# Kernel optimization log

Hardware: AMD Instinct MI355X
Metric: run time of the kernel (lower is better)

The kernel has to match this reference:

```python
import jax, jax.numpy as jnp
import numpy as np

N = 50000       # nodes
E = 100000      # edges (avg degree ~2 per direction, molecular graphs)
EDGE_DIM = 8
EH = 32         # edge-MLP hidden width
DIN = 32
H1, H2 = 32, 64
NGRAPH = 256
EPS = 1e-5


def setup_inputs():
    key = jax.random.key(0)
    ks = jax.random.split(key, 16)
    def rn(k, shape, fan):
        return jax.random.normal(k, shape, jnp.float32) * np.float32(1.0 / np.sqrt(fan))
    return {
        "x": jax.random.normal(ks[0], (N, DIN), jnp.float32),
        "edge_index": jax.random.randint(ks[1], (2, E), 0, N),
        "edge_attr": jax.random.uniform(ks[2], (E, EDGE_DIM), jnp.float32),
        "batch_index": jnp.sort(jax.random.randint(ks[3], (N,), 0, NGRAPH)),
        # NNConv layer 1: DIN -> H1
        "e1_w1": rn(ks[4], (EDGE_DIM, EH), EDGE_DIM), "e1_b1": jnp.zeros((EH,), jnp.float32),
        "e1_w2": rn(ks[5], (EH, DIN * H1), EH), "e1_b2": jnp.zeros((DIN * H1,), jnp.float32),
        "root1": rn(ks[6], (DIN, H1), DIN), "bias1": jnp.zeros((H1,), jnp.float32),
        # NNConv layer 2: H1 -> H2
        "e2_w1": rn(ks[7], (EDGE_DIM, EH), EDGE_DIM), "e2_b1": jnp.zeros((EH,), jnp.float32),
        "e2_w2": rn(ks[8], (EH, H1 * H2), EH), "e2_b2": jnp.zeros((H1 * H2,), jnp.float32),
        "root2": rn(ks[9], (H1, H2), H1), "bias2": jnp.zeros((H2,), jnp.float32),
        # MLP head
        "h1_w": rn(ks[10], (2 * H2, H2), 2 * H2), "h1_b": jnp.zeros((H2,), jnp.float32),
        "bn1_g": jnp.ones((H2,), jnp.float32), "bn1_b": jnp.zeros((H2,), jnp.float32),
        "bn1_m": jnp.zeros((H2,), jnp.float32), "bn1_v": jnp.ones((H2,), jnp.float32),
        "h2_w": rn(ks[11], (H2, H2 // 2), H2), "h2_b": jnp.zeros((H2 // 2,), jnp.float32),
        "bn2_g": jnp.ones((H2 // 2,), jnp.float32), "bn2_b": jnp.zeros((H2 // 2,), jnp.float32),
        "bn2_m": jnp.zeros((H2 // 2,), jnp.float32), "bn2_v": jnp.ones((H2 // 2,), jnp.float32),
        "h3_w": rn(ks[12], (H2 // 2, 1), H2 // 2), "h3_b": jnp.zeros((1,), jnp.float32),
    }


def nnconv_layer(x, src, dst, edge_attr, w1, b1, w2, b2, root, bias, din, dout):
    # edge MLP -> per-edge weight matrix [E, din, dout]
    h = jax.nn.relu(edge_attr @ w1 + b1)
    W = (h @ w2 + b2).reshape(-1, din, dout)
    # gather source features, per-edge matmul, scatter-add to targets
    msg = jnp.einsum('ei,eio->eo', x[src], W)
    agg = jax.ops.segment_sum(msg, dst, num_segments=x.shape[0])
    return x @ root + agg + bias


def bn_eval(x, g, b, m, v):
    return (x - m) * jax.lax.rsqrt(v + EPS) * g + b


def reference(x, edge_index, edge_attr, batch_index,
              e1_w1, e1_b1, e1_w2, e1_b2, root1, bias1,
              e2_w1, e2_b1, e2_w2, e2_b2, root2, bias2,
              h1_w, h1_b, bn1_g, bn1_b, bn1_m, bn1_v,
              h2_w, h2_b, bn2_g, bn2_b, bn2_m, bn2_v,
              h3_w, h3_b):
    src, dst = edge_index[0], edge_index[1]
    h = nnconv_layer(x, src, dst, edge_attr, e1_w1, e1_b1, e1_w2, e1_b2, root1, bias1, DIN, H1)
    h = jax.nn.relu(h)
    h = nnconv_layer(h, src, dst, edge_attr, e2_w1, e2_b1, e2_w2, e2_b2, root2, bias2, H1, H2)
    # global max + mean pool per graph
    gmax = jax.ops.segment_max(h, batch_index, num_segments=NGRAPH)
    cnt = jax.ops.segment_sum(jnp.ones((h.shape[0],), h.dtype), batch_index, num_segments=NGRAPH)
    gmean = jax.ops.segment_sum(h, batch_index, num_segments=NGRAPH) / jnp.maximum(cnt, 1.0)[:, None]
    feat = jnp.concatenate([gmax, gmean], axis=1)  # [NGRAPH, 2*H2]
    # MLP head (eval mode: BN uses running stats, dropout = identity)
    z = jax.nn.relu(bn_eval(feat @ h1_w + h1_b, bn1_g, bn1_b, bn1_m, bn1_v))
    z = jax.nn.relu(bn_eval(z @ h2_w + h2_b, bn2_g, bn2_b, bn2_m, bn2_v))
    return z @ h3_w + h3_b
```

## Files before the change

### kernel.cpp

```cpp
#include <hip/hip_runtime.h>
#include <hip/hip_fp16.h>

#define N_NODES 50000
#define N_EDGES 100000
#define EDGE_DIM 8
#define EHID 32
#define DIN 32
#define H1 32
#define H2 64
#define NGRAPH 256
#define BN_EPS 1e-5f
#define KTOT 1056

#define EH_BLOCKS  ((N_EDGES + 255) / 256)
#define PREP_TOTAL ((H1 + H2) * KTOT)
#define PREP_BLOCKS (PREP_TOTAL / 256)
#define INIT_BLOCKS 253
#define MSG_BLOCKS 512

typedef __attribute__((ext_vector_type(8))) _Float16 f16x8;
typedef __attribute__((ext_vector_type(4))) float f32x4;
typedef unsigned int uint32;

__device__ inline void atomicMaxF(float* addr, float v) {
    if (v >= 0.0f) atomicMax((int*)addr, __float_as_int(v));
    else           atomicMin((unsigned int*)addr, __float_as_uint(v));
}

__device__ inline uint32 pk_f16(float a, float b) {
    uint32 r;
    asm("v_cvt_pkrtz_f16_f32 %0, %1, %2" : "=v"(r) : "v"(a), "v"(b));
    return r;
}

union GF { uint32 u[4]; f16x8 v; };

__device__ inline f16x8 mul_h(uint32 h, const GF& g) {
    GF r;
    asm("v_pk_mul_f16 %0, %1, %2" : "=v"(r.u[0]) : "v"(h), "v"(g.u[0]));
    asm("v_pk_mul_f16 %0, %1, %2" : "=v"(r.u[1]) : "v"(h), "v"(g.u[1]));
    asm("v_pk_mul_f16 %0, %1, %2" : "=v"(r.u[2]) : "v"(h), "v"(g.u[2]));
    asm("v_pk_mul_f16 %0, %1, %2" : "=v"(r.u[3]) : "v"(h), "v"(g.u[3]));
    return r.v;
}

__global__ __launch_bounds__(256) void prologue_kernel(
    const float* __restrict__ edge_attr,
    const float* __restrict__ e1w1, const float* __restrict__ e1b1,
    const float* __restrict__ e2w1, const float* __restrict__ e2b1,
    const float* __restrict__ e1w2, const float* __restrict__ e1b2,
    const float* __restrict__ e2w2, const float* __restrict__ e2b2,
    uint32* __restrict__ hpk1, uint32* __restrict__ hpk2,
    unsigned short* __restrict__ w2h1, unsigned short* __restrict__ w2h2,
    float* __restrict__ agg1, float* __restrict__ agg2,
    float* __restrict__ gmax, float* __restrict__ gsum, float* __restrict__ gcnt)
{
    int bid = blockIdx.x, tid = threadIdx.x;
    if (bid < EH_BLOCKS) {
        __shared__ float s_w[2][EDGE_DIM * EHID];
        __shared__ float s_b[2][EHID];
        if (tid < EDGE_DIM * EHID) { s_w[0][tid] = e1w1[tid]; s_w[1][tid] = e2w1[tid]; }
        if (tid < EHID) { s_b[0][tid] = e1b1[tid]; s_b[1][tid] = e2b1[tid]; }
        __syncthreads();
        int e = bid * 256 + tid;
        if (e >= N_EDGES) return;
        const float4* eap = reinterpret_cast<const float4*>(edge_attr + (size_t)e * EDGE_DIM);
        float4 v0 = eap[0], v1 = eap[1];
        float ea[EDGE_DIM] = {v0.x, v0.y, v0.z, v0.w, v1.x, v1.y, v1.z, v1.w};
#pragma unroll
        for (int L = 0; L < 2; ++L) {
            uint32* hp = (L == 0 ? hpk1 : hpk2) + (size_t)e * EHID;
#pragma unroll
            for (int k4 = 0; k4 < EHID; k4 += 4) {
                uint32 t[4];
#pragma unroll
                for (int q = 0; q < 4; ++q) {
                    int k = k4 + q;
                    float acc = s_b[L][k];
#pragma unroll
                    for (int j = 0; j < EDGE_DIM; ++j) acc += ea[j] * s_w[L][j * EHID + k];
                    acc = fmaxf(acc, 0.0f);
                    t[q] = pk_f16(acc, acc);
                }
                uint4 r; r.x = t[0]; r.y = t[1]; r.z = t[2]; r.w = t[3];
                *reinterpret_cast<uint4*>(hp + k4) = r;
            }
        }
    } else if (bid < EH_BLOCKS + PREP_BLOCKS) {
        int idx = (bid - EH_BLOCKS) * 256 + tid;
        const int n1 = H1 * KTOT;
        if (idx < n1) {
            int o = idx / KTOT, k = idx % KTOT;
            float v = (k < EHID * DIN) ? e1w2[(k >> 5) * (DIN * H1) + (k & 31) * H1 + o]
                                       : e1b2[(k - EHID * DIN) * H1 + o];
            w2h1[idx] = __half_as_ushort(__float2half(v));
        } else {
            int j = idx - n1;
            int o = j / KTOT, k = j % KTOT;
            float v = (k < EHID * DIN) ? e2w2[(k >> 5) * (DIN * H2) + (k & 31) * H2 + o]
                                       : e2b2[(k - EHID * DIN) * H2 + o];
            w2h2[j] = __half_as_ushort(__float2half(v));
        }
    } else {
        int lb = bid - EH_BLOCKS - PREP_BLOCKS;
        int stride = INIT_BLOCKS * 256;
        int i0 = lb * 256 + tid;
        for (int i = i0; i < N_NODES * H1; i += stride) agg1[i] = 0.0f;
        for (int i = i0; i < N_NODES * H2; i += stride) agg2[i] = 0.0f;
        for (int i = i0; i < NGRAPH * H2; i += stride) { gmax[i] = __int_as_float(0xff800000); gsum[i] = 0.0f; }
        for (int i = i0; i < NGRAPH; i += stride) gcnt[i] = 0.0f;
    }
}

template <int DOUT>
__global__ __launch_bounds__(256, 2) void msg_v4_kernel(
    const float* __restrict__ gsrc,
    const uint32* __restrict__ hpk,
    const int* __restrict__ src, const int* __restrict__ dst,
    const unsigned short* __restrict__ w2h,
    float* __restrict__ agg)
{
    constexpr int NT = DOUT / 16;
    __shared__ __align__(16) uint32 hlds[4][2][32][36];

    const int tid = threadIdx.x;
    const int wave = tid >> 6;
    const int lane = tid & 63;
    const int col = lane & 15;
    const int kq = lane >> 4;

    const int w = blockIdx.x * 4 + wave;
    const int ot = w % NT;
    int it = w / NT;
    const int strideIt = (MSG_BLOCKS * 4) / NT;
    const int NIT = N_EDGES / 32;

    f16x8 B[33];
    {
        const unsigned short* bp = w2h + (size_t)(ot * 16 + col) * KTOT + kq * 8;
#pragma unroll
        for (int kk = 0; kk < 33; ++kk)
            B[kk] = *reinterpret_cast<const f16x8*>(bp + kk * 32);
    }
    if (it >= NIT) return;

    int buf = 0;

    int e0 = it * 32;
    int sA = src[e0 + col], sB = src[e0 + 16 + col];
    float4 gA0 = *reinterpret_cast<const float4*>(gsrc + (size_t)sA * DIN + kq * 8);
    float4 gA1 = *reinterpret_cast<const float4*>(gsrc + (size_t)sA * DIN + kq * 8 + 4);
    float4 gB0 = *reinterpret_cast<const float4*>(gsrc + (size_t)sB * DIN + kq * 8);
    float4 gB1 = *reinterpret_cast<const float4*>(gsrc + (size_t)sB * DIN + kq * 8 + 4);
    uint4 hA0 = *reinterpret_cast<const uint4*>(hpk + (size_t)(e0 + col) * EHID + kq * 8);
    uint4 hA1 = *reinterpret_cast<const uint4*>(hpk + (size_t)(e0 + col) * EHID + kq * 8 + 4);
    uint4 hB0 = *reinterpret_cast<const uint4*>(hpk + (size_t)(e0 + 16 + col) * EHID + kq * 8);
    uint4 hB1 = *reinterpret_cast<const uint4*>(hpk + (size_t)(e0 + 16 + col) * EHID + kq * 8 + 4);
    int4 ddA = *reinterpret_cast<const int4*>(dst + e0 + kq * 4);
    int4 ddB = *reinterpret_cast<const int4*>(dst + e0 + 16 + kq * 4);

    int it1 = it + strideIt;
    int s1A = 0, s1B = 0;
    if (it1 < NIT) { s1A = src[it1 * 32 + col]; s1B = src[it1 * 32 + 16 + col]; }

    GF gfA, gfB;
    gfA.u[0] = pk_f16(gA0.x, gA0.y); gfA.u[1] = pk_f16(gA0.z, gA0.w);
    gfA.u[2] = pk_f16(gA1.x, gA1.y); gfA.u[3] = pk_f16(gA1.z, gA1.w);
    gfB.u[0] = pk_f16(gB0.x, gB0.y); gfB.u[1] = pk_f16(gB0.z, gB0.w);
    gfB.u[2] = pk_f16(gB1.x, gB1.y); gfB.u[3] = pk_f16(gB1.z, gB1.w);
    *reinterpret_cast<uint4*>(&hlds[wave][0][col][kq * 8])          = hA0;
    *reinterpret_cast<uint4*>(&hlds[wave][0][col][kq * 8 + 4])      = hA1;
    *reinterpret_cast<uint4*>(&hlds[wave][0][16 + col][kq * 8])     = hB0;
    *reinterpret_cast<uint4*>(&hlds[wave][0][16 + col][kq * 8 + 4]) = hB1;

    for (;;) {
        int it2 = it1 + strideIt;
        int s2A = 0, s2B = 0;
        if (it2 < NIT) { s2A = src[it2 * 32 + col]; s2B = src[it2 * 32 + 16 + col]; }

        const bool nv = (it1 < NIT);
        float4 ngA0, ngA1, ngB0, ngB1;
        uint4 nhA0, nhA1, nhB0, nhB1;
        int4 nddA, nddB;
        if (nv) {
            int ne0 = it1 * 32;
            ngA0 = *reinterpret_cast<const float4*>(gsrc + (size_t)s1A * DIN + kq * 8);
            ngA1 = *reinterpret_cast<const float4*>(gsrc + (size_t)s1A * DIN + kq * 8 + 4);
            ngB0 = *reinterpret_cast<const float4*>(gsrc + (size_t)s1B * DIN + kq * 8);
            ngB1 = *reinterpret_cast<const float4*>(gsrc + (size_t)s1B * DIN + kq * 8 + 4);
            nhA0 = *reinterpret_cast<const uint4*>(hpk + (size_t)(ne0 + col) * EHID + kq * 8);
            nhA1 = *reinterpret_cast<const uint4*>(hpk + (size_t)(ne0 + col) * EHID + kq * 8 + 4);
            nhB0 = *reinterpret_cast<const uint4*>(hpk + (size_t)(ne0 + 16 + col) * EHID + kq * 8);
            nhB1 = *reinterpret_cast<const uint4*>(hpk + (size_t)(ne0 + 16 + col) * EHID + kq * 8 + 4);
            nddA = *reinterpret_cast<const int4*>(dst + ne0 + kq * 4);
            nddB = *reinterpret_cast<const int4*>(dst + ne0 + 16 + kq * 4);
        }

        f32x4 accA = (f32x4){0.f, 0.f, 0.f, 0.f};
        f32x4 accB = (f32x4){0.f, 0.f, 0.f, 0.f};
#pragma unroll
        for (int t = 0; t < 8; ++t) {
            uint4 ha = *reinterpret_cast<const uint4*>(&hlds[wave][buf][col][t * 4]);
            uint4 hb = *reinterpret_cast<const uint4*>(&hlds[wave][buf][16 + col][t * 4]);
            accA = __builtin_amdgcn_mfma_f32_16x16x32_f16(mul_h(ha.x, gfA), B[t * 4 + 0], accA, 0, 0, 0);
            accB = __builtin_amdgcn_mfma_f32_16x16x32_f16(mul_h(hb.x, gfB), B[t * 4 + 0], accB, 0, 0, 0);
            accA = __builtin_amdgcn_mfma_f32_16x16x32_f16(mul_h(ha.y, gfA), B[t * 4 + 1], accA, 0, 0, 0);
            accB = __builtin_amdgcn_mfma_f32_16x16x32_f16(mul_h(hb.y, gfB), B[t * 4 + 1], accB, 0, 0, 0);
            accA = __builtin_amdgcn_mfma_f32_16x16x32_f16(mul_h(ha.z, gfA), B[t * 4 + 2], accA, 0, 0, 0);
            accB = __builtin_amdgcn_mfma_f32_16x16x32_f16(mul_h(hb.z, gfB), B[t * 4 + 2], accB, 0, 0, 0);
            accA = __builtin_amdgcn_mfma_f32_16x16x32_f16(mul_h(ha.w, gfA), B[t * 4 + 3], accA, 0, 0, 0);
            accB = __builtin_amdgcn_mfma_f32_16x16x32_f16(mul_h(hb.w, gfB), B[t * 4 + 3], accB, 0, 0, 0);
        }
        accA = __builtin_amdgcn_mfma_f32_16x16x32_f16(gfA.v, B[32], accA, 0, 0, 0);
        accB = __builtin_amdgcn_mfma_f32_16x16x32_f16(gfB.v, B[32], accB, 0, 0, 0);

        atomicAdd(&agg[(size_t)ddA.x * DOUT + ot * 16 + col], accA[0]);
        atomicAdd(&agg[(size_t)ddA.y * DOUT + ot * 16 + col], accA[1]);
        atomicAdd(&agg[(size_t)ddA.z * DOUT + ot * 16 + col], accA[2]);
        atomicAdd(&agg[(size_t)ddA.w * DOUT + ot * 16 + col], accA[3]);
        atomicAdd(&agg[(size_t)ddB.x * DOUT + ot * 16 + col], accB[0]);
        atomicAdd(&agg[(size_t)ddB.y * DOUT + ot * 16 + col], accB[1]);
        atomicAdd(&agg[(size_t)ddB.z * DOUT + ot * 16 + col], accB[2]);
        atomicAdd(&agg[(size_t)ddB.w * DOUT + ot * 16 + col], accB[3]);

        if (!nv) break;

        buf ^= 1;
        *reinterpret_cast<uint4*>(&hlds[wave][buf][col][kq * 8])          = nhA0;
        *reinterpret_cast<uint4*>(&hlds[wave][buf][col][kq * 8 + 4])      = nhA1;
        *reinterpret_cast<uint4*>(&hlds[wave][buf][16 + col][kq * 8])     = nhB0;
        *reinterpret_cast<uint4*>(&hlds[wave][buf][16 + col][kq * 8 + 4]) = nhB1;
        gfA.u[0] = pk_f16(ngA0.x, ngA0.y); gfA.u[1] = pk_f16(ngA0.z, ngA0.w);
        gfA.u[2] = pk_f16(ngA1.x, ngA1.y); gfA.u[3] = pk_f16(ngA1.z, ngA1.w);
        gfB.u[0] = pk_f16(ngB0.x, ngB0.y); gfB.u[1] = pk_f16(ngB0.z, ngB0.w);
        gfB.u[2] = pk_f16(ngB1.x, ngB1.y); gfB.u[3] = pk_f16(ngB1.z, ngB1.w);
        ddA = nddA; ddB = nddB;
        s1A = s2A; s1B = s2B;
        it = it1; it1 = it2;
    }
}

template <int DOUTN, bool RELU>
__global__ __launch_bounds__(256) void node_update_kernel(
    const float* __restrict__ in, const float* __restrict__ root,
    const float* __restrict__ agg, const float* __restrict__ bias,
    float* __restrict__ out)
{
    constexpr int NPB = 256 / DOUTN;
    __shared__ float roots[DIN * DOUTN];
    __shared__ float ins[NPB][DIN + 1];
    int tid = threadIdx.x;
    for (int idx = tid; idx < DIN * DOUTN; idx += 256) roots[idx] = root[idx];
    int o = tid % DOUTN, nl = tid / DOUTN;
    float bo = bias[o];
    const int nchunks = (N_NODES + NPB - 1) / NPB;
    for (int c = blockIdx.x; c < nchunks; c += gridDim.x) {
        int nBase = c * NPB;
        __syncthreads();
        for (int idx = tid; idx < NPB * DIN; idx += 256) {
            int nn = nBase + idx / DIN;
            ins[idx / DIN][idx % DIN] = (nn < N_NODES) ? in[(size_t)nn * DIN + (idx % DIN)] : 0.0f;
        }
        __syncthreads();
        int n = nBase + nl;
        if (n < N_NODES) {
            float t = agg[(size_t)n * DOUTN + o] + bo;
#pragma unroll
            for (int i = 0; i < DIN; ++i) t += ins[nl][i] * roots[i * DOUTN + o];
            if (RELU) t = fmaxf(t, 0.0f);
            out[(size_t)n * DOUTN + o] = t;
        }
    }
}

__global__ __launch_bounds__(256) void pool_scan_kernel(
    const float* __restrict__ h, const int* __restrict__ batch,
    float* gmax, float* gsum, float* gcnt)
{
    __shared__ int s_batch[64];
    int tid = threadIdx.x;
    int base = blockIdx.x * 64;
    if (tid < 64) s_batch[tid] = (base + tid < N_NODES) ? batch[base + tid] : -1;
    __syncthreads();
    int o = tid & 63, r = tid >> 6;
    int curb = -1; float s = 0.f, m = __int_as_float(0xff800000); float c = 0.f;
#pragma unroll
    for (int j = 0; j < 16; ++j) {
        int n = base + r * 16 + j;
        if (n >= N_NODES) break;
        int b = s_batch[r * 16 + j];
        if (b != curb) {
            if (curb >= 0) {
                atomicAdd(&gsum[curb * H2 + o], s);
                atomicMaxF(&gmax[curb * H2 + o], m);
                if (o == 0) atomicAdd(&gcnt[curb], c);
            }
            curb = b; s = 0.f; m = __int_as_float(0xff800000); c = 0.f;
        }
        float v = h[(size_t)n * H2 + o];
        s += v; m = fmaxf(m, v); c += 1.f;
    }
    if (curb >= 0) {
        atomicAdd(&gsum[curb * H2 + o], s);
        atomicMaxF(&gmax[curb * H2 + o], m);
        if (o == 0) atomicAdd(&gcnt[curb], c);
    }
}

__global__ __launch_bounds__(128) void head_kernel(
    const float* __restrict__ gmax, const float* __restrict__ gsum, const float* __restrict__ gcnt,
    const float* __restrict__ h1w, const float* __restrict__ h1b,
    const float* __restrict__ bn1g, const float* __restrict__ bn1b,
    const float* __restrict__ bn1m, const float* __restrict__ bn1v,
    const float* __restrict__ h2w, const float* __restrict__ h2b,
    const float* __restrict__ bn2g, const float* __restrict__ bn2b,
    const float* __restrict__ bn2m, const float* __restrict__ bn2v,
    const float* __restrict__ h3w, const float* __restrict__ h3b,
    float* __restrict__ out)
{
    __shared__ float feat[2 * H2];
    __shared__ float z1s[H2];
    __shared__ float z2s[H2 / 2];
    int b = blockIdx.x, tid = threadIdx.x;
    float cnt = fmaxf(gcnt[b], 1.0f);
    if (tid < H2) feat[tid] = gmax[b * H2 + tid];
    else          feat[tid] = gsum[b * H2 + (tid - H2)] / cnt;
    __syncthreads();
    if (tid < H2) {
        float acc = h1b[tid];
#pragma unroll
        for (int j = 0; j < 2 * H2; ++j) acc += feat[j] * h1w[j * H2 + tid];
        acc = (acc - bn1m[tid]) * rsqrtf(bn1v[tid] + BN_EPS) * bn1g[tid] + bn1b[tid];
        z1s[tid] = fmaxf(acc, 0.0f);
    }
    __syncthreads();
    if (tid < H2 / 2) {
        float acc = h2b[tid];
#pragma unroll
        for (int j = 0; j < H2; ++j) acc += z1s[j] * h2w[j * (H2 / 2) + tid];
        acc = (acc - bn2m[tid]) * rsqrtf(bn2v[tid] + BN_EPS) * bn2g[tid] + bn2b[tid];
        z2s[tid] = fmaxf(acc, 0.0f);
    }
    __syncthreads();
    if (tid == 0) {
        float acc = h3b[0];
#pragma unroll
        for (int j = 0; j < H2 / 2; ++j) acc += z2s[j] * h3w[j];
        out[b] = acc;
    }
}

extern "C" void kernel_launch(void* const* d_in, const int* in_sizes, int n_in,
                              void* d_out, int out_size, void* d_ws, size_t ws_size,
                              hipStream_t stream)
{
    const float* x         = (const float*)d_in[0];
    const int*   ei        = (const int*)d_in[1];
    const float* edge_attr = (const float*)d_in[2];
    const int*   batch     = (const int*)d_in[3];
    const float* e1_w1 = (const float*)d_in[4];
    const float* e1_b1 = (const float*)d_in[5];
    const float* e1_w2 = (const float*)d_in[6];
    const float* e1_b2 = (const float*)d_in[7];
    const float* root1 = (const float*)d_in[8];
    const float* bias1 = (const float*)d_in[9];
    const float* e2_w1 = (const float*)d_in[10];
    const float* e2_b1 = (const float*)d_in[11];
    const float* e2_w2 = (const float*)d_in[12];
    const float* e2_b2 = (const float*)d_in[13];
    const float* root2 = (const float*)d_in[14];
    const float* bias2 = (const float*)d_in[15];
    const float* h1w = (const float*)d_in[16];
    const float* h1b = (const float*)d_in[17];
    const float* bn1g = (const float*)d_in[18];
    const float* bn1b = (const float*)d_in[19];
    const float* bn1m = (const float*)d_in[20];
    const float* bn1v = (const float*)d_in[21];
    const float* h2w = (const float*)d_in[22];
    const float* h2b = (const float*)d_in[23];
    const float* bn2g = (const float*)d_in[24];
    const float* bn2b = (const float*)d_in[25];
    const float* bn2m = (const float*)d_in[26];
    const float* bn2v = (const float*)d_in[27];
    const float* h3w = (const float*)d_in[28];
    const float* h3b = (const float*)d_in[29];
    float* out = (float*)d_out;

    float* ws = (float*)d_ws;
    uint32* hpk1 = (uint32*)ws;
    uint32* hpk2 = hpk1 + (size_t)N_EDGES * EHID;
    float* out1  = (float*)(hpk2 + (size_t)N_EDGES * EHID);
    float* agg1  = out1 + (size_t)N_NODES * H1;
    float* agg2  = agg1 + (size_t)N_NODES * H1;
    float* gmaxb = agg2 + (size_t)N_NODES * H2;
    float* gsumb = gmaxb + NGRAPH * H2;
    float* gcntb = gsumb + NGRAPH * H2;
    unsigned short* w2h1 = (unsigned short*)(gcntb + 256);
    unsigned short* w2h2 = w2h1 + (size_t)H1 * KTOT;
    float* h2o = (float*)hpk1;

    const int* srcp = ei;
    const int* dstp = ei + N_EDGES;

    prologue_kernel<<<EH_BLOCKS + PREP_BLOCKS + INIT_BLOCKS, 256, 0, stream>>>(
        edge_attr, e1_w1, e1_b1, e2_w1, e2_b1, e1_w2, e1_b2, e2_w2, e2_b2,
        hpk1, hpk2, w2h1, w2h2, agg1, agg2, gmaxb, gsumb, gcntb);

    msg_v4_kernel<H1><<<MSG_BLOCKS, 256, 0, stream>>>(x, hpk1, srcp, dstp, w2h1, agg1);
    node_update_kernel<H1, true><<<2048, 256, 0, stream>>>(x, root1, agg1, bias1, out1);

    msg_v4_kernel<H2><<<MSG_BLOCKS, 256, 0, stream>>>(out1, hpk2, srcp, dstp, w2h2, agg2);
    node_update_kernel<H2, false><<<2048, 256, 0, stream>>>(out1, root2, agg2, bias2, h2o);

    pool_scan_kernel<<<(N_NODES + 63) / 64, 256, 0, stream>>>(h2o, batch, gmaxb, gsumb, gcntb);
    head_kernel<<<NGRAPH, 128, 0, stream>>>(gmaxb, gsumb, gcntb,
                                            h1w, h1b, bn1g, bn1b, bn1m, bn1v,
                                            h2w, h2b, bn2g, bn2b, bn2m, bn2v,
                                            h3w, h3b, out);
}
```

Measured before the change: 116.9 us.

## Replace atomic scatter-add with per-edge message buffers and CSR-style gather

```diff
diff --git a/kernel.cpp b/kernel.cpp
--- a/kernel.cpp
+++ b/kernel.cpp
@@ -11,11 +11,12 @@
 #define NGRAPH 256
 #define BN_EPS 1e-5f
 #define KTOT 1056
+#define MAXDEG 32
 
 #define EH_BLOCKS  ((N_EDGES + 255) / 256)
 #define PREP_TOTAL ((H1 + H2) * KTOT)
 #define PREP_BLOCKS (PREP_TOTAL / 256)
-#define INIT_BLOCKS 253
+#define INIT_BLOCKS 16
 #define MSG_BLOCKS 512
 
 typedef __attribute__((ext_vector_type(8))) _Float16 f16x8;
@@ -45,14 +46,14 @@
 }
 
 __global__ __launch_bounds__(256) void prologue_kernel(
-    const float* __restrict__ edge_attr,
+    const float* __restrict__ edge_attr, const int* __restrict__ dstp,
     const float* __restrict__ e1w1, const float* __restrict__ e1b1,
     const float* __restrict__ e2w1, const float* __restrict__ e2b1,
     const float* __restrict__ e1w2, const float* __restrict__ e1b2,
     const float* __restrict__ e2w2, const float* __restrict__ e2b2,
     uint32* __restrict__ hpk1, uint32* __restrict__ hpk2,
     unsigned short* __restrict__ w2h1, unsigned short* __restrict__ w2h2,
-    float* __restrict__ agg1, float* __restrict__ agg2,
+    int* __restrict__ deg, int* __restrict__ etab,
     float* __restrict__ gmax, float* __restrict__ gsum, float* __restrict__ gcnt)
 {
     int bid = blockIdx.x, tid = threadIdx.x;
@@ -64,6 +65,9 @@
         __syncthreads();
         int e = bid * 256 + tid;
         if (e >= N_EDGES) return;
+        int d = dstp[e];
+        int slot = atomicAdd(&deg[d], 1);
+        if (slot < MAXDEG) etab[(size_t)d * MAXDEG + slot] = e;
         const float4* eap = reinterpret_cast<const float4*>(edge_attr + (size_t)e * EDGE_DIM);
         float4 v0 = eap[0], v1 = eap[1];
         float ea[EDGE_DIM] = {v0.x, v0.y, v0.z, v0.w, v1.x, v1.y, v1.z, v1.w};
@@ -105,20 +109,18 @@
         int lb = bid - EH_BLOCKS - PREP_BLOCKS;
         int stride = INIT_BLOCKS * 256;
         int i0 = lb * 256 + tid;
-        for (int i = i0; i < N_NODES * H1; i += stride) agg1[i] = 0.0f;
-        for (int i = i0; i < N_NODES * H2; i += stride) agg2[i] = 0.0f;
         for (int i = i0; i < NGRAPH * H2; i += stride) { gmax[i] = __int_as_float(0xff800000); gsum[i] = 0.0f; }
         for (int i = i0; i < NGRAPH; i += stride) gcnt[i] = 0.0f;
     }
 }
 
 template <int DOUT>
-__global__ __launch_bounds__(256, 2) void msg_v4_kernel(
+__global__ __launch_bounds__(256, 2) void msg_v5_kernel(
     const float* __restrict__ gsrc,
     const uint32* __restrict__ hpk,
-    const int* __restrict__ src, const int* __restrict__ dst,
+    const int* __restrict__ src,
     const unsigned short* __restrict__ w2h,
-    float* __restrict__ agg)
+    float* __restrict__ msg)
 {
     constexpr int NT = DOUT / 16;
     __shared__ __align__(16) uint32 hlds[4][2][32][36];
@@ -156,8 +158,6 @@
     uint4 hA1 = *reinterpret_cast<const uint4*>(hpk + (size_t)(e0 + col) * EHID + kq * 8 + 4);
     uint4 hB0 = *reinterpret_cast<const uint4*>(hpk + (size_t)(e0 + 16 + col) * EHID + kq * 8);
     uint4 hB1 = *reinterpret_cast<const uint4*>(hpk + (size_t)(e0 + 16 + col) * EHID + kq * 8 + 4);
-    int4 ddA = *reinterpret_cast<const int4*>(dst + e0 + kq * 4);
-    int4 ddB = *reinterpret_cast<const int4*>(dst + e0 + 16 + kq * 4);
 
     int it1 = it + strideIt;
     int s1A = 0, s1B = 0;
@@ -181,7 +181,6 @@
         const bool nv = (it1 < NIT);
         float4 ngA0, ngA1, ngB0, ngB1;
         uint4 nhA0, nhA1, nhB0, nhB1;
-        int4 nddA, nddB;
         if (nv) {
             int ne0 = it1 * 32;
             ngA0 = *reinterpret_cast<const float4*>(gsrc + (size_t)s1A * DIN + kq * 8);
@@ -192,8 +191,6 @@
             nhA1 = *reinterpret_cast<const uint4*>(hpk + (size_t)(ne0 + col) * EHID + kq * 8 + 4);
             nhB0 = *reinterpret_cast<const uint4*>(hpk + (size_t)(ne0 + 16 + col) * EHID + kq * 8);
             nhB1 = *reinterpret_cast<const uint4*>(hpk + (size_t)(ne0 + 16 + col) * EHID + kq * 8 + 4);
-            nddA = *reinterpret_cast<const int4*>(dst + ne0 + kq * 4);
-            nddB = *reinterpret_cast<const int4*>(dst + ne0 + 16 + kq * 4);
         }
 
         f32x4 accA = (f32x4){0.f, 0.f, 0.f, 0.f};
@@ -214,14 +211,15 @@
         accA = __builtin_amdgcn_mfma_f32_16x16x32_f16(gfA.v, B[32], accA, 0, 0, 0);
         accB = __builtin_amdgcn_mfma_f32_16x16x32_f16(gfB.v, B[32], accB, 0, 0, 0);
 
-        atomicAdd(&agg[(size_t)ddA.x * DOUT + ot * 16 + col], accA[0]);
-        atomicAdd(&agg[(size_t)ddA.y * DOUT + ot * 16 + col], accA[1]);
-        atomicAdd(&agg[(size_t)ddA.z * DOUT + ot * 16 + col], accA[2]);
-        atomicAdd(&agg[(size_t)ddA.w * DOUT + ot * 16 + col], accA[3]);
-        atomicAdd(&agg[(size_t)ddB.x * DOUT + ot * 16 + col], accB[0]);
-        atomicAdd(&agg[(size_t)ddB.y * DOUT + ot * 16 + col], accB[1]);
-        atomicAdd(&agg[(size_t)ddB.z * DOUT + ot * 16 + col], accB[2]);
-        atomicAdd(&agg[(size_t)ddB.w * DOUT + ot * 16 + col], accB[3]);
+        {
+            const int oc = ot * 16 + col;
+#pragma unroll
+            for (int r = 0; r < 4; ++r)
+                msg[(size_t)(e0 + kq * 4 + r) * DOUT + oc] = accA[r];
+#pragma unroll
+            for (int r = 0; r < 4; ++r)
+                msg[(size_t)(e0 + 16 + kq * 4 + r) * DOUT + oc] = accB[r];
+        }
 
         if (!nv) break;
 
@@ -234,16 +232,17 @@
         gfA.u[2] = pk_f16(ngA1.x, ngA1.y); gfA.u[3] = pk_f16(ngA1.z, ngA1.w);
         gfB.u[0] = pk_f16(ngB0.x, ngB0.y); gfB.u[1] = pk_f16(ngB0.z, ngB0.w);
         gfB.u[2] = pk_f16(ngB1.x, ngB1.y); gfB.u[3] = pk_f16(ngB1.z, ngB1.w);
-        ddA = nddA; ddB = nddB;
         s1A = s2A; s1B = s2B;
+        e0 = it1 * 32;
         it = it1; it1 = it2;
     }
 }
 
 template <int DOUTN, bool RELU>
-__global__ __launch_bounds__(256) void node_update_kernel(
+__global__ __launch_bounds__(256) void gather_update_kernel(
     const float* __restrict__ in, const float* __restrict__ root,
-    const float* __restrict__ agg, const float* __restrict__ bias,
+    const float* __restrict__ msg, const int* __restrict__ deg,
+    const int* __restrict__ etab, const float* __restrict__ bias,
     float* __restrict__ out)
 {
     constexpr int NPB = 256 / DOUTN;
@@ -264,9 +263,15 @@
         __syncthreads();
         int n = nBase + nl;
         if (n < N_NODES) {
-            float t = agg[(size_t)n * DOUTN + o] + bo;
+            float t = bo;
 #pragma unroll
             for (int i = 0; i < DIN; ++i) t += ins[nl][i] * roots[i * DOUTN + o];
+            int dg = deg[n]; if (dg > MAXDEG) dg = MAXDEG;
+            const int* ep = etab + (size_t)n * MAXDEG;
+            for (int j = 0; j < dg; ++j) {
+                int e = ep[j];
+                t += msg[(size_t)e * DOUTN + o];
+            }
             if (RELU) t = fmaxf(t, 0.0f);
             out[(size_t)n * DOUTN + o] = t;
         }
@@ -389,28 +394,32 @@
     float* ws = (float*)d_ws;
     uint32* hpk1 = (uint32*)ws;
     uint32* hpk2 = hpk1 + (size_t)N_EDGES * EHID;
-    float* out1  = (float*)(hpk2 + (size_t)N_EDGES * EHID);
-    float* agg1  = out1 + (size_t)N_NODES * H1;
-    float* agg2  = agg1 + (size_t)N_NODES * H1;
-    float* gmaxb = agg2 + (size_t)N_NODES * H2;
+    float* msg1  = (float*)(hpk2 + (size_t)N_EDGES * EHID);
+    float* msg2  = msg1 + (size_t)N_EDGES * H1;
+    float* out1  = msg2 + (size_t)N_EDGES * H2;
+    float* h2o   = out1 + (size_t)N_NODES * H1;
+    float* gmaxb = h2o + (size_t)N_NODES * H2;
     float* gsumb = gmaxb + NGRAPH * H2;
     float* gcntb = gsumb + NGRAPH * H2;
-    unsigned short* w2h1 = (unsigned short*)(gcntb + 256);
+    int*   degp  = (int*)(gcntb + 256);
+    int*   etab  = degp + N_NODES;
+    unsigned short* w2h1 = (unsigned short*)(etab + (size_t)N_NODES * MAXDEG);
     unsigned short* w2h2 = w2h1 + (size_t)H1 * KTOT;
-    float* h2o = (float*)hpk1;
 
     const int* srcp = ei;
     const int* dstp = ei + N_EDGES;
 
+    hipMemsetAsync(degp, 0, (size_t)N_NODES * sizeof(int), stream);
+
     prologue_kernel<<<EH_BLOCKS + PREP_BLOCKS + INIT_BLOCKS, 256, 0, stream>>>(
-        edge_attr, e1_w1, e1_b1, e2_w1, e2_b1, e1_w2, e1_b2, e2_w2, e2_b2,
-        hpk1, hpk2, w2h1, w2h2, agg1, agg2, gmaxb, gsumb, gcntb);
-
-    msg_v4_kernel<H1><<<MSG_BLOCKS, 256, 0, stream>>>(x, hpk1, srcp, dstp, w2h1, agg1);
-    node_update_kernel<H1, true><<<2048, 256, 0, stream>>>(x, root1, agg1, bias1, out1);
-
-    msg_v4_kernel<H2><<<MSG_BLOCKS, 256, 0, stream>>>(out1, hpk2, srcp, dstp, w2h2, agg2);
-    node_update_kernel<H2, false><<<2048, 256, 0, stream>>>(out1, root2, agg2, bias2, h2o);
+        edge_attr, dstp, e1_w1, e1_b1, e2_w1, e2_b1, e1_w2, e1_b2, e2_w2, e2_b2,
+        hpk1, hpk2, w2h1, w2h2, degp, etab, gmaxb, gsumb, gcntb);
+
+    msg_v5_kernel<H1><<<MSG_BLOCKS, 256, 0, stream>>>(x, hpk1, srcp, w2h1, msg1);
+    gather_update_kernel<H1, true><<<1024, 256, 0, stream>>>(x, root1, msg1, degp, etab, bias1, out1);
+
+    msg_v5_kernel<H2><<<MSG_BLOCKS, 256, 0, stream>>>(out1, hpk2, srcp, w2h2, msg2);
+    gather_update_kernel<H2, false><<<1024, 256, 0, stream>>>(out1, root2, msg2, degp, etab, bias2, h2o);
 
     pool_scan_kernel<<<(N_NODES + 63) / 64, 256, 0, stream>>>(h2o, batch, gmaxb, gsumb, gcntb);
     head_kernel<<<NGRAPH, 128, 0, stream>>>(gmaxb, gsumb, gcntb,
```

After: 147.6 us. +26.3%, slower.

## Fold node-update kernels into prologue, message and pooling kernels

Applied to the files above, without the earlier changes.

```diff
diff --git a/kernel.cpp b/kernel.cpp
--- a/kernel.cpp
+++ b/kernel.cpp
@@ -15,7 +15,8 @@
 #define EH_BLOCKS  ((N_EDGES + 255) / 256)
 #define PREP_TOTAL ((H1 + H2) * KTOT)
 #define PREP_BLOCKS (PREP_TOTAL / 256)
-#define INIT_BLOCKS 253
+#define NU1_BLOCKS 512
+#define INIT_BLOCKS 128
 #define MSG_BLOCKS 512
 
 typedef __attribute__((ext_vector_type(8))) _Float16 f16x8;
@@ -34,6 +35,18 @@
 }
 
 union GF { uint32 u[4]; f16x8 v; };
+
+template <bool RELUG>
+__device__ inline GF pack_g8(float4 a, float4 b) {
+    if (RELUG) {
+        a.x = fmaxf(a.x, 0.f); a.y = fmaxf(a.y, 0.f); a.z = fmaxf(a.z, 0.f); a.w = fmaxf(a.w, 0.f);
+        b.x = fmaxf(b.x, 0.f); b.y = fmaxf(b.y, 0.f); b.z = fmaxf(b.z, 0.f); b.w = fmaxf(b.w, 0.f);
+    }
+    GF gf;
+    gf.u[0] = pk_f16(a.x, a.y); gf.u[1] = pk_f16(a.z, a.w);
+    gf.u[2] = pk_f16(b.x, b.y); gf.u[3] = pk_f16(b.z, b.w);
+    return gf;
+}
 
 __device__ inline f16x8 mul_h(uint32 h, const GF& g) {
     GF r;
@@ -50,6 +63,8 @@
     const float* __restrict__ e2w1, const float* __restrict__ e2b1,
     const float* __restrict__ e1w2, const float* __restrict__ e1b2,
     const float* __restrict__ e2w2, const float* __restrict__ e2b2,
+    const float* __restrict__ x, const float* __restrict__ root1,
+    const float* __restrict__ bias1,
     uint32* __restrict__ hpk1, uint32* __restrict__ hpk2,
     unsigned short* __restrict__ w2h1, unsigned short* __restrict__ w2h2,
     float* __restrict__ agg1, float* __restrict__ agg2,
@@ -101,19 +116,40 @@
                                        : e2b2[(k - EHID * DIN) * H2 + o];
             w2h2[j] = __half_as_ushort(__float2half(v));
         }
+    } else if (bid < EH_BLOCKS + PREP_BLOCKS + NU1_BLOCKS) {
+        __shared__ float roots[DIN * H1];
+        __shared__ float ins[8][DIN + 1];
+        int lb = bid - EH_BLOCKS - PREP_BLOCKS;
+        for (int idx = tid; idx < DIN * H1; idx += 256) roots[idx] = root1[idx];
+        int o = tid & 31, nl = tid >> 5;
+        float bo = bias1[o];
+        const int nch = N_NODES / 8;
+        for (int c = lb; c < nch; c += NU1_BLOCKS) {
+            __syncthreads();
+            for (int idx = tid; idx < 8 * DIN; idx += 256)
+                ins[idx >> 5][idx & 31] = x[(size_t)(c * 8 + (idx >> 5)) * DIN + (idx & 31)];
+            __syncthreads();
+            int n = c * 8 + nl;
+            float t = bo;
+#pragma unroll
+            for (int i = 0; i < DIN; ++i) t += ins[nl][i] * roots[i * H1 + o];
+            agg1[(size_t)n * H1 + o] = t;
+        }
     } else {
-        int lb = bid - EH_BLOCKS - PREP_BLOCKS;
+        int lb = bid - EH_BLOCKS - PREP_BLOCKS - NU1_BLOCKS;
         int stride = INIT_BLOCKS * 256;
         int i0 = lb * 256 + tid;
-        for (int i = i0; i < N_NODES * H1; i += stride) agg1[i] = 0.0f;
-        for (int i = i0; i < N_NODES * H2; i += stride) agg2[i] = 0.0f;
+        float4* a2 = (float4*)agg2;
+        const int n4 = N_NODES * H2 / 4;
+        float4 z4 = {0.f, 0.f, 0.f, 0.f};
+        for (int i = i0; i < n4; i += stride) a2[i] = z4;
         for (int i = i0; i < NGRAPH * H2; i += stride) { gmax[i] = __int_as_float(0xff800000); gsum[i] = 0.0f; }
         for (int i = i0; i < NGRAPH; i += stride) gcnt[i] = 0.0f;
     }
 }
 
-template <int DOUT>
-__global__ __launch_bounds__(256, 2) void msg_v4_kernel(
+template <int DOUT, bool RELUG>
+__global__ __launch_bounds__(256, 2) void msg_v6_kernel(
     const float* __restrict__ gsrc,
     const uint32* __restrict__ hpk,
     const int* __restrict__ src, const int* __restrict__ dst,
@@ -163,11 +199,8 @@
     int s1A = 0, s1B = 0;
     if (it1 < NIT) { s1A = src[it1 * 32 + col]; s1B = src[it1 * 32 + 16 + col]; }
 
-    GF gfA, gfB;
-    gfA.u[0] = pk_f16(gA0.x, gA0.y); gfA.u[1] = pk_f16(gA0.z, gA0.w);
-    gfA.u[2] = pk_f16(gA1.x, gA1.y); gfA.u[3] = pk_f16(gA1.z, gA1.w);
-    gfB.u[0] = pk_f16(gB0.x, gB0.y); gfB.u[1] = pk_f16(gB0.z, gB0.w);
-    gfB.u[2] = pk_f16(gB1.x, gB1.y); gfB.u[3] = pk_f16(gB1.z, gB1.w);
+    GF gfA = pack_g8<RELUG>(gA0, gA1);
+    GF gfB = pack_g8<RELUG>(gB0, gB1);
     *reinterpret_cast<uint4*>(&hlds[wave][0][col][kq * 8])          = hA0;
     *reinterpret_cast<uint4*>(&hlds[wave][0][col][kq * 8 + 4])      = hA1;
     *reinterpret_cast<uint4*>(&hlds[wave][0][16 + col][kq * 8])     = hB0;
@@ -214,14 +247,15 @@
         accA = __builtin_amdgcn_mfma_f32_16x16x32_f16(gfA.v, B[32], accA, 0, 0, 0);
         accB = __builtin_amdgcn_mfma_f32_16x16x32_f16(gfB.v, B[32], accB, 0, 0, 0);
 
-        atomicAdd(&agg[(size_t)ddA.x * DOUT + ot * 16 + col], accA[0]);
-        atomicAdd(&agg[(size_t)ddA.y * DOUT + ot * 16 + col], accA[1]);
-        atomicAdd(&agg[(size_t)ddA.z * DOUT + ot * 16 + col], accA[2]);
-        atomicAdd(&agg[(size_t)ddA.w * DOUT + ot * 16 + col], accA[3]);
-        atomicAdd(&agg[(size_t)ddB.x * DOUT + ot * 16 + col], accB[0]);
-        atomicAdd(&agg[(size_t)ddB.y * DOUT + ot * 16 + col], accB[1]);
-        atomicAdd(&agg[(size_t)ddB.z * DOUT + ot * 16 + col], accB[2]);
-        atomicAdd(&agg[(size_t)ddB.w * DOUT + ot * 16 + col], accB[3]);
+        const int oc = ot * 16 + col;
+        atomicAdd(&agg[(size_t)ddA.x * DOUT + oc], accA[0]);
+        atomicAdd(&agg[(size_t)ddA.y * DOUT + oc], accA[1]);
+        atomicAdd(&agg[(size_t)ddA.z * DOUT + oc], accA[2]);
+        atomicAdd(&agg[(size_t)ddA.w * DOUT + oc], accA[3]);
+        atomicAdd(&agg[(size_t)ddB.x * DOUT + oc], accB[0]);
+        atomicAdd(&agg[(size_t)ddB.y * DOUT + oc], accB[1]);
+        atomicAdd(&agg[(size_t)ddB.z * DOUT + oc], accB[2]);
+        atomicAdd(&agg[(size_t)ddB.w * DOUT + oc], accB[3]);
 
         if (!nv) break;
 
@@ -230,65 +264,41 @@
         *reinterpret_cast<uint4*>(&hlds[wave][buf][col][kq * 8 + 4])      = nhA1;
         *reinterpret_cast<uint4*>(&hlds[wave][buf][16 + col][kq * 8])     = nhB0;
         *reinterpret_cast<uint4*>(&hlds[wave][buf][16 + col][kq * 8 + 4]) = nhB1;
-        gfA.u[0] = pk_f16(ngA0.x, ngA0.y); gfA.u[1] = pk_f16(ngA0.z, ngA0.w);
-        gfA.u[2] = pk_f16(ngA1.x, ngA1.y); gfA.u[3] = pk_f16(ngA1.z, ngA1.w);
-        gfB.u[0] = pk_f16(ngB0.x, ngB0.y); gfB.u[1] = pk_f16(ngB0.z, ngB0.w);
-        gfB.u[2] = pk_f16(ngB1.x, ngB1.y); gfB.u[3] = pk_f16(ngB1.z, ngB1.w);
+        gfA = pack_g8<RELUG>(ngA0, ngA1);
+        gfB = pack_g8<RELUG>(ngB0, ngB1);
         ddA = nddA; ddB = nddB;
         s1A = s2A; s1B = s2B;
         it = it1; it1 = it2;
     }
 }
 
-template <int DOUTN, bool RELU>
-__global__ __launch_bounds__(256) void node_update_kernel(
-    const float* __restrict__ in, const float* __restrict__ root,
-    const float* __restrict__ agg, const float* __restrict__ bias,
-    float* __restrict__ out)
-{
-    constexpr int NPB = 256 / DOUTN;
-    __shared__ float roots[DIN * DOUTN];
-    __shared__ float ins[NPB][DIN + 1];
-    int tid = threadIdx.x;
-    for (int idx = tid; idx < DIN * DOUTN; idx += 256) roots[idx] = root[idx];
-    int o = tid % DOUTN, nl = tid / DOUTN;
-    float bo = bias[o];
-    const int nchunks = (N_NODES + NPB - 1) / NPB;
-    for (int c = blockIdx.x; c < nchunks; c += gridDim.x) {
-        int nBase = c * NPB;
-        __syncthreads();
-        for (int idx = tid; idx < NPB * DIN; idx += 256) {
-            int nn = nBase + idx / DIN;
-            ins[idx / DIN][idx % DIN] = (nn < N_NODES) ? in[(size_t)nn * DIN + (idx % DIN)] : 0.0f;
-        }
-        __syncthreads();
-        int n = nBase + nl;
-        if (n < N_NODES) {
-            float t = agg[(size_t)n * DOUTN + o] + bo;
-#pragma unroll
-            for (int i = 0; i < DIN; ++i) t += ins[nl][i] * roots[i * DOUTN + o];
-            if (RELU) t = fmaxf(t, 0.0f);
-            out[(size_t)n * DOUTN + o] = t;
-        }
-    }
-}
-
-__global__ __launch_bounds__(256) void pool_scan_kernel(
-    const float* __restrict__ h, const int* __restrict__ batch,
+__global__ __launch_bounds__(256) void update2_pool_kernel(
+    const float* __restrict__ agg1, const float* __restrict__ root2,
+    const float* __restrict__ agg2, const float* __restrict__ bias2,
+    const int* __restrict__ batch,
     float* gmax, float* gsum, float* gcnt)
 {
-    __shared__ int s_batch[64];
+    __shared__ float a1[64][DIN + 1];
+    __shared__ float r2[DIN * H2];
+    __shared__ int bt[64];
     int tid = threadIdx.x;
     int base = blockIdx.x * 64;
-    if (tid < 64) s_batch[tid] = (base + tid < N_NODES) ? batch[base + tid] : -1;
+    for (int idx = tid; idx < DIN * H2; idx += 256) r2[idx] = root2[idx];
+    for (int idx = tid; idx < 64 * DIN; idx += 256) {
+        int nn = base + (idx >> 5);
+        a1[idx >> 5][idx & 31] = (nn < N_NODES) ? fmaxf(agg1[(size_t)nn * DIN + (idx & 31)], 0.0f) : 0.0f;
+    }
+    if (tid < 64) bt[tid] = (base + tid < N_NODES) ? batch[base + tid] : -1;
     __syncthreads();
+
     int o = tid & 63, r = tid >> 6;
+    float bo = bias2[o];
     int curb = -1; float s = 0.f, m = __int_as_float(0xff800000); float c = 0.f;
 #pragma unroll
     for (int j = 0; j < 16; ++j) {
         int n = base + r * 16 + j;
         if (n >= N_NODES) break;
-        int b = s_batch[r * 16 + j];
+        int b = bt[r * 16 + j];
         if (b != curb) {
             if (curb >= 0) {
                 atomicAdd(&gsum[curb * H2 + o], s);
@@ -297,7 +307,9 @@
             }
             curb = b; s = 0.f; m = __int_as_float(0xff800000); c = 0.f;
         }
-        float v = h[(size_t)n * H2 + o];
+        float v = bo + agg2[(size_t)n * H2 + o];
+#pragma unroll
+        for (int i = 0; i < DIN; ++i) v += a1[r * 16 + j][i] * r2[i * H2 + o];
         s += v; m = fmaxf(m, v); c += 1.f;
     }
     if (curb >= 0) {
@@ -389,30 +401,28 @@
     float* ws = (float*)d_ws;
     uint32* hpk1 = (uint32*)ws;
     uint32* hpk2 = hpk1 + (size_t)N_EDGES * EHID;
-    float* out1  = (float*)(hpk2 + (size_t)N_EDGES * EHID);
-    float* agg1  = out1 + (size_t)N_NODES * H1;
+    float* agg1  = (float*)(hpk2 + (size_t)N_EDGES * EHID);
     float* agg2  = agg1 + (size_t)N_NODES * H1;
     float* gmaxb = agg2 + (size_t)N_NODES * H2;
     float* gsumb = gmaxb + NGRAPH * H2;
     float* gcntb = gsumb + NGRAPH * H2;
     unsigned short* w2h1 = (unsigned short*)(gcntb + 256);
     unsigned short* w2h2 = w2h1 + (size_t)H1 * KTOT;
-    float* h2o = (float*)hpk1;
 
     const int* srcp = ei;
     const int* dstp = ei + N_EDGES;
 
-    prologue_kernel<<<EH_BLOCKS + PREP_BLOCKS + INIT_BLOCKS, 256, 0, stream>>>(
+    prologue_kernel<<<EH_BLOCKS + PREP_BLOCKS + NU1_BLOCKS + INIT_BLOCKS, 256, 0, stream>>>(
         edge_attr, e1_w1, e1_b1, e2_w1, e2_b1, e1_w2, e1_b2, e2_w2, e2_b2,
+        x, root1, bias1,
         hpk1, hpk2, w2h1, w2h2, agg1, agg2, gmaxb, gsumb, gcntb);
 
-    msg_v4_kernel<H1><<<MSG_BLOCKS, 256, 0, stream>>>(x, hpk1, srcp, dstp, w2h1, agg1);
-    node_update_kernel<H1, true><<<2048, 256, 0, stream>>>(x, root1, agg1, bias1, out1);
-
-    msg_v4_kernel<H2><<<MSG_BLOCKS, 256, 0, stream>>>(out1, hpk2, srcp, dstp, w2h2, agg2);
-    node_update_kernel<H2, false><<<2048, 256, 0, stream>>>(out1, root2, agg2, bias2, h2o);
-
-    pool_scan_kernel<<<(N_NODES + 63) / 64, 256, 0, stream>>>(h2o, batch, gmaxb, gsumb, gcntb);
+    msg_v6_kernel<H1, false><<<MSG_BLOCKS, 256, 0, stream>>>(x, hpk1, srcp, dstp, w2h1, agg1);
+    msg_v6_kernel<H2, true><<<MSG_BLOCKS, 256, 0, stream>>>(agg1, hpk2, srcp, dstp, w2h2, agg2);
+
+    update2_pool_kernel<<<(N_NODES + 63) / 64, 256, 0, stream>>>(
+        agg1, root2, agg2, bias2, batch, gmaxb, gsumb, gcntb);
+
     head_kernel<<<NGRAPH, 128, 0, stream>>>(gmaxb, gsumb, gcntb,
                                             h1w, h1b, bn1g, bn1b, bn1m, bn1v,
                                             h2w, h2b, bn2g, bn2b, bn2m, bn2v,
```

Result: faster. 109.6 us (-6.2%).
